# Performance work log

Measured on AMD Instinct MI355X. Metric: run time of the kernel, lower is better.

The kernel has to match this reference:

```python
import jax, jax.numpy as jnp
import numpy as np

N_NODES = 100000
N_EDGES = 3200000
N_GRAPHS = 256
IN_DIM = 128
HID = 64
K = 3


def setup_inputs() -> dict:
    key = jax.random.key(0)
    ks = jax.random.split(key, 10)
    x = jax.random.normal(ks[0], (N_NODES, IN_DIM), dtype=jnp.float32)
    edge_index = jax.random.randint(ks[1], (2, N_EDGES), 0, N_NODES, dtype=jnp.int64)
    batch = jnp.sort(jax.random.randint(ks[2], (N_NODES,), 0, N_GRAPHS, dtype=jnp.int64))
    # ChebConv k-order weights: list of Linear(in, out) -> stacked [K, in, out]
    s1 = 1.0 / np.sqrt(IN_DIM)
    s2 = 1.0 / np.sqrt(HID)
    W1 = jax.random.uniform(ks[3], (K, IN_DIM, HID), jnp.float32, -s1, s1)
    b1 = jax.random.uniform(ks[4], (HID,), jnp.float32, -s1, s1)
    W2 = jax.random.uniform(ks[5], (K, HID, HID), jnp.float32, -s2, s2)
    b2 = jax.random.uniform(ks[6], (HID,), jnp.float32, -s2, s2)
    Wfc = jax.random.uniform(ks[7], (HID, 1), jnp.float32, -s2, s2)
    bfc = jax.random.uniform(ks[8], (1,), jnp.float32, -s2, s2)
    return {"x": x, "edge_index": edge_index, "batch": batch,
            "W1": W1, "b1": b1, "W2": W2, "b2": b2, "Wfc": Wfc, "bfc": bfc}


def _cheb_conv(x, src, dst, edge_w, W, b):
    # PyG ChebConv, sym normalization, lambda_max=2 => L_hat has zero diagonal
    # and off-diagonal -D^{-1/2} A D^{-1/2} (edge_w precomputed, negative).
    n = x.shape[0]
    def lhat(v):  # (L_hat v)_i = sum_{edges j->i} edge_w * v_j
        return jax.ops.segment_sum(edge_w[:, None] * v[src], dst, num_segments=n)
    Tx0 = x
    Tx1 = lhat(Tx0)
    Tx2 = 2.0 * lhat(Tx1) - Tx0
    return Tx0 @ W[0] + Tx1 @ W[1] + Tx2 @ W[2] + b


def reference(x, edge_index, batch, W1, b1, W2, b2, Wfc, bfc):
    src, dst = edge_index[0], edge_index[1]
    n = x.shape[0]
    # degree on row (source), sym normalization
    deg = jax.ops.segment_sum(jnp.ones_like(src, dtype=x.dtype), src, num_segments=n)
    dinv = jnp.where(deg > 0, jax.lax.rsqrt(jnp.maximum(deg, 1.0)), 0.0)
    edge_w = -dinv[src] * dinv[dst]  # scaled Laplacian off-diagonal weights

    h = jax.nn.relu(_cheb_conv(x, src, dst, edge_w, W1, b1))
    h = jax.nn.relu(_cheb_conv(h, src, dst, edge_w, W2, b2))

    # global mean pool over graphs
    sums = jax.ops.segment_sum(h, batch, num_segments=N_GRAPHS)
    counts = jax.ops.segment_sum(jnp.ones((n,), dtype=h.dtype), batch, num_segments=N_GRAPHS)
    pooled = sums / jnp.maximum(counts, 1.0)[:, None]

    return (pooled @ Wfc + bfc).squeeze(-1)  # [N_GRAPHS]
```

## Files before the change

### kernel.cpp

```cpp
#include <hip/hip_runtime.h>
#include <hip/hip_fp16.h>
#include <cstdint>
#include <cstddef>

static constexpr int NN = 100000;
static constexpr int NE = 3200000;
static constexpr int NG = 256;
static constexpr int NBK = (NN + 127) / 128;
static constexpr int EPB = NE / 256;
static constexpr int GB_BATCH = (NN + 255) / 256;
static constexpr int GB_PREPW = (192 * 128 + 192 * 64 + 255) / 256;
static constexpr int GB_HIST = 256;

typedef _Float16 h8 __attribute__((ext_vector_type(8)));
typedef float f4v __attribute__((ext_vector_type(4)));

__device__ __forceinline__ void atomAddF(float* p, float v) {
  unsafeAtomicAdd(p, v);
}
__device__ __forceinline__ float h2f(__half h) { return __half2float(h); }

__global__ void k_detect(const int* __restrict__ ei, int* __restrict__ flag) {
  if (threadIdx.x == 0 && blockIdx.x == 0) {
    int nz = 0;
    for (int i = 0; i < 64; ++i) nz += (ei[2 * i + 1] != 0) ? 1 : 0;
    *flag = (nz == 0) ? 1 : 0;
  }
}

__device__ __forceinline__ int ld_idx(const void* raw, int f, int i) {
  return f ? (int)((const long long*)raw)[i] : ((const int*)raw)[i];
}

__global__ __launch_bounds__(256) void k_front(const void* __restrict__ bat,
                                               const void* __restrict__ ei,
                                               const int* __restrict__ flag,
                                               const float* __restrict__ W1,
                                               const float* __restrict__ W2,
                                               int* __restrict__ b32,
                                               int* __restrict__ gcnt,
                                               __half* __restrict__ BtX,
                                               __half* __restrict__ BtH2,
                                               int* __restrict__ sCnt,
                                               int* __restrict__ dCnt,
                                               int* __restrict__ hsBlk,
                                               int* __restrict__ hdBlk) {
  __shared__ int sh[2 * NBK];
  int b = blockIdx.x;
  int t = threadIdx.x;
  if (b < GB_BATCH) {
    int* cnt = sh;
    cnt[t] = 0;
    int blk0 = b * 256;
    int f = *flag;
    int g0 = ld_idx(bat, f, blk0);
    __syncthreads();
    int i = blk0 + t;
    if (i < NN) {
      int g = ld_idx(bat, f, i);
      b32[i] = g;
      atomicAdd(&cnt[g - g0], 1);
    }
    __syncthreads();
    if (cnt[t] > 0) atomicAdd(&gcnt[g0 + t], cnt[t]);
  } else if (b < GB_BATCH + GB_PREPW) {
    int u = (b - GB_BATCH) * 256 + t;
    if (u < 192 * 128) {
      int n = u >> 7, k = u & 127;
      float v;
      if (n < 64)       v = W1[k * 64 + n] - W1[16384 + k * 64 + n];
      else if (n < 128) v = W1[8192 + k * 64 + (n - 64)];
      else              v = W1[16384 + k * 64 + (n - 128)];
      BtX[n * 128 + k] = __float2half_rn(v);
    } else if (u < 192 * 128 + 192 * 64) {
      int u2 = u - 192 * 128;
      int n = u2 >> 6, k = u2 & 63;
      float v;
      if (n < 64)       v = W2[k * 64 + n] - W2[8192 + k * 64 + n];
      else if (n < 128) v = W2[4096 + k * 64 + (n - 64)];
      else              v = W2[8192 + k * 64 + (n - 128)];
      BtH2[n * 64 + k] = __float2half_rn(v);
    }
  } else {
    int hb = b - GB_BATCH - GB_PREPW;
    int* hs = sh;
    int* hd = sh + NBK;
    for (int i = t; i < NBK; i += 256) { hs[i] = 0; hd[i] = 0; }
    __syncthreads();
    int f = *flag;
    int e0 = hb * EPB;
    for (int e = e0 + t; e < e0 + EPB; e += 256) {
      int s = ld_idx(ei, f, e);
      int d = ld_idx(ei, f, NE + e);
      atomicAdd(&hs[s >> 7], 1);
      atomicAdd(&hd[d >> 7], 1);
    }
    __syncthreads();
    size_t hoff = (size_t)hb * NBK;
    for (int i = t; i < NBK; i += 256) {
      int a = hs[i], c = hd[i];
      hsBlk[hoff + i] = a;
      hdBlk[hoff + i] = c;
      if (a) atomicAdd(&sCnt[i], a);
      if (c) atomicAdd(&dCnt[i], c);
    }
  }
}

__global__ __launch_bounds__(1024) void k_scan(const int* __restrict__ sCnt,
                                               const int* __restrict__ dCnt,
                                               int* __restrict__ sBase,
                                               int* __restrict__ dBase,
                                               int* __restrict__ sCur,
                                               int* __restrict__ dCur) {
  __shared__ int sh1[1024], sh2[1024];
  int t = threadIdx.x;
  int v1 = (t < NBK) ? sCnt[t] : 0;
  int v2 = (t < NBK) ? dCnt[t] : 0;
  sh1[t] = v1; sh2[t] = v2;
  __syncthreads();
  for (int off = 1; off < 1024; off <<= 1) {
    int a1 = (t >= off) ? sh1[t - off] : 0;
    int a2 = (t >= off) ? sh2[t - off] : 0;
    __syncthreads();
    sh1[t] += a1; sh2[t] += a2;
    __syncthreads();
  }
  if (t <= NBK) {
    int b1 = sh1[t] - v1, b2 = sh2[t] - v2;
    sBase[t] = b1; dBase[t] = b2;
    if (t < NBK) { sCur[t] = b1; dCur[t] = b2; }
  }
}

__global__ __launch_bounds__(256) void k_scatter(const void* __restrict__ raw,
                                                 const int* __restrict__ flag,
                                                 const int* __restrict__ hsBlk,
                                                 const int* __restrict__ hdBlk,
                                                 int* __restrict__ sCur,
                                                 int* __restrict__ dCur,
                                                 int* __restrict__ srclist,
                                                 unsigned* __restrict__ elist) {
  __shared__ int hs[NBK], hd[NBK], cbS[NBK], cbD[NBK];
  int t = threadIdx.x;
  size_t hb = (size_t)blockIdx.x * NBK;
  for (int i = t; i < NBK; i += 256) {
    int c1 = hsBlk[hb + i];
    cbS[i] = c1 ? atomicAdd(&sCur[i], c1) : 0;
    int c2 = hdBlk[hb + i];
    cbD[i] = c2 ? atomicAdd(&dCur[i], c2) : 0;
    hs[i] = 0; hd[i] = 0;
  }
  __syncthreads();
  int f = *flag;
  int e0 = blockIdx.x * EPB;
  for (int e = e0 + t; e < e0 + EPB; e += 256) {
    int s = ld_idx(raw, f, e);
    int d = ld_idx(raw, f, NE + e);
    int bs = s >> 7, bd = d >> 7;
    int ls = atomicAdd(&hs[bs], 1);
    int ld2 = atomicAdd(&hd[bd], 1);
    srclist[cbS[bs] + ls] = s;
    elist[cbD[bd] + ld2] = (unsigned)s | ((unsigned)(d & 127) << 17);
  }
}

__global__ __launch_bounds__(256) void k_back(const int* __restrict__ sBase,
                                              const int* __restrict__ srclist,
                                              float* __restrict__ dinv,
                                              const int* __restrict__ dBase,
                                              const unsigned* __restrict__ elist,
                                              int* __restrict__ rowptr,
                                              int* __restrict__ adj) {
  __shared__ int cnt[128], sc[128], off[128], fill[128];
  int t = threadIdx.x;
  int bb = blockIdx.x;
  if (bb < NBK) {
    int b = bb;
    if (t < 128) cnt[t] = 0;
    __syncthreads();
    int e0 = sBase[b], e1 = sBase[b + 1];
    for (int i = e0 + t; i < e1; i += 256) atomicAdd(&cnt[srclist[i] & 127], 1);
    __syncthreads();
    if (t < 128) {
      int node = b * 128 + t;
      if (node < NN) {
        int c = cnt[t];
        dinv[node] = (c > 0) ? rsqrtf((float)c) : 0.f;
      }
    }
  } else {
    int b = bb - NBK;
    if (t < 128) { cnt[t] = 0; fill[t] = 0; }
    __syncthreads();
    int e0 = dBase[b], e1 = dBase[b + 1];
    for (int i = e0 + t; i < e1; i += 256) atomicAdd(&cnt[elist[i] >> 17], 1);
    __syncthreads();
    if (t < 128) sc[t] = cnt[t];
    __syncthreads();
    for (int o = 1; o < 128; o <<= 1) {
      int a = (t < 128 && t >= o) ? sc[t - o] : 0;
      __syncthreads();
      if (t < 128) sc[t] += a;
      __syncthreads();
    }
    if (t < 128) {
      off[t] = sc[t] - cnt[t];
      int node = b * 128 + t;
      if (node < NN) rowptr[node] = e0 + off[t];
    }
    if (b == NBK - 1 && t == 0) rowptr[NN] = e1;
    __syncthreads();
    for (int i = e0 + t; i < e1; i += 256) {
      unsigned w2 = elist[i];
      int l = (int)(w2 >> 17);
      int pos = atomicAdd(&fill[l], 1);
      adj[e0 + off[l] + pos] = (int)(w2 & 0x1FFFFu);
    }
  }
}

static constexpr int AW = 136;
__global__ __launch_bounds__(256) void k_gemm_x(const float* __restrict__ x,
                                                const __half* __restrict__ BtX,
                                                const float* __restrict__ dinv,
                                                __half* __restrict__ gV0,
                                                __half* __restrict__ gA1,
                                                __half* __restrict__ gU2s) {
  __shared__ __align__(16) _Float16 As[128 * AW];
  const int t = threadIdx.x;
  const int n0 = blockIdx.x * 128;
  {
    int i = t >> 1, q = t & 1;
    int row = n0 + i;
    _Float16* dst = As + i * AW + q * 64;
    if (row < NN) {
      const float* src = x + (size_t)row * 128 + q * 64;
#pragma unroll
      for (int c = 0; c < 64; c += 4) {
        float4 v = *reinterpret_cast<const float4*>(src + c);
        ushort4 u;
        u.x = __half_as_ushort(__float2half_rn(v.x));
        u.y = __half_as_ushort(__float2half_rn(v.y));
        u.z = __half_as_ushort(__float2half_rn(v.z));
        u.w = __half_as_ushort(__float2half_rn(v.w));
        *reinterpret_cast<ushort4*>(dst + c) = u;
      }
    } else {
#pragma unroll
      for (int c = 0; c < 64; c += 4)
        *reinterpret_cast<ushort4*>(dst + c) = make_ushort4(0, 0, 0, 0);
    }
  }
  __syncthreads();
  const int w = t >> 6, lane = t & 63;
  const int quad = lane >> 4, l = lane & 15;
  f4v acc[2][12];
#pragma unroll
  for (int mt = 0; mt < 2; ++mt)
#pragma unroll
    for (int nt = 0; nt < 12; ++nt) acc[mt][nt] = (f4v){0.f, 0.f, 0.f, 0.f};

#pragma unroll
  for (int ks = 0; ks < 4; ++ks) {
    int k0 = ks * 32 + quad * 8;
    h8 a0 = *reinterpret_cast<const h8*>(As + (w * 32 + l) * AW + k0);
    h8 a1 = *reinterpret_cast<const h8*>(As + (w * 32 + 16 + l) * AW + k0);
#pragma unroll
    for (int nt = 0; nt < 12; ++nt) {
      h8 b = *reinterpret_cast<const h8*>(BtX + (size_t)(nt * 16 + l) * 128 + k0);
      acc[0][nt] = __builtin_amdgcn_mfma_f32_16x16x32_f16(a0, b, acc[0][nt], 0, 0, 0);
      acc[1][nt] = __builtin_amdgcn_mfma_f32_16x16x32_f16(a1, b, acc[1][nt], 0, 0, 0);
    }
  }
#pragma unroll
  for (int mt = 0; mt < 2; ++mt) {
#pragma unroll
    for (int r = 0; r < 4; ++r) {
      int row = n0 + w * 32 + mt * 16 + quad * 4 + r;
      if (row < NN) {
        float dv = dinv[row];
#pragma unroll
        for (int nt2 = 0; nt2 < 4; ++nt2) {
          int col = nt2 * 16 + l;
          gV0[(size_t)row * 64 + col] = __float2half_rn(acc[mt][nt2][r]);
          gA1[(size_t)row * 64 + col] = __float2half_rn(acc[mt][4 + nt2][r]);
          gU2s[(size_t)row * 64 + col] = __float2half_rn(dv * acc[mt][8 + nt2][r]);
        }
      }
    }
  }
}

static constexpr int HW2 = 72;
__global__ __launch_bounds__(256) void k_gemm_h(const __half* __restrict__ gH1,
                                                const __half* __restrict__ BtH2,
                                                const float* __restrict__ dinv,
                                                __half* __restrict__ gV02,
                                                __half* __restrict__ gA2,
                                                __half* __restrict__ gB2s) {
  __shared__ __align__(16) _Float16 As[128 * HW2];
  const int t = threadIdx.x;
  const int n0 = blockIdx.x * 128;
  for (int c = t; c < 128 * 8; c += 256) {
    int row = c >> 3, seg = c & 7;
    int rowg = n0 + row;
    h8 v = (h8){0, 0, 0, 0, 0, 0, 0, 0};
    if (rowg < NN) v = *reinterpret_cast<const h8*>(gH1 + (size_t)rowg * 64 + seg * 8);
    *reinterpret_cast<h8*>(As + row * HW2 + seg * 8) = v;
  }
  __syncthreads();
  const int w = t >> 6, lane = t & 63;
  const int quad = lane >> 4, l = lane & 15;
  f4v acc[2][12];
#pragma unroll
  for (int mt = 0; mt < 2; ++mt)
#pragma unroll
    for (int nt = 0; nt < 12; ++nt) acc[mt][nt] = (f4v){0.f, 0.f, 0.f, 0.f};
#pragma unroll
  for (int ks = 0; ks < 2; ++ks) {
    int k0 = ks * 32 + quad * 8;
    h8 a0 = *reinterpret_cast<const h8*>(As + (w * 32 + l) * HW2 + k0);
    h8 a1 = *reinterpret_cast<const h8*>(As + (w * 32 + 16 + l) * HW2 + k0);
#pragma unroll
    for (int nt = 0; nt < 12; ++nt) {
      h8 b = *reinterpret_cast<const h8*>(BtH2 + (size_t)(nt * 16 + l) * 64 + k0);
      acc[0][nt] = __builtin_amdgcn_mfma_f32_16x16x32_f16(a0, b, acc[0][nt], 0, 0, 0);
      acc[1][nt] = __builtin_amdgcn_mfma_f32_16x16x32_f16(a1, b, acc[1][nt], 0, 0, 0);
    }
  }
#pragma unroll
  for (int mt = 0; mt < 2; ++mt) {
#pragma unroll
    for (int r = 0; r < 4; ++r) {
      int row = n0 + w * 32 + mt * 16 + quad * 4 + r;
      if (row < NN) {
        float dv = dinv[row];
#pragma unroll
        for (int nt2 = 0; nt2 < 4; ++nt2) {
          int col = nt2 * 16 + l;
          gV02[(size_t)row * 64 + col] = __float2half_rn(acc[mt][nt2][r]);
          gA2[(size_t)row * 64 + col] = __float2half_rn(acc[mt][4 + nt2][r]);
          gB2s[(size_t)row * 64 + col] = __float2half_rn(dv * acc[mt][8 + nt2][r]);
        }
      }
    }
  }
}

#define GATHER_SUM(tbl)                                                    \
  int p0 = rp[node], p1 = rp[node + 1];                                    \
  float a0 = 0.f, a1 = 0.f, a2 = 0.f, a3 = 0.f;                            \
  float a4 = 0.f, a5 = 0.f, a6 = 0.f, a7 = 0.f;                            \
  int p = p0;                                                              \
  int pA = (p0 + 3) & ~3;                                                  \
  if (pA > p1) pA = p1;                                                    \
  for (; p < pA; ++p) a0 += h2f(tbl[(size_t)adj[p] * 64 + d]);             \
  for (; p + 16 <= p1; p += 16) {                                          \
    int4 e0 = *reinterpret_cast<const int4*>(adj + p);                     \
    int4 e1 = *reinterpret_cast<const int4*>(adj + p + 4);                 \
    int4 e2 = *reinterpret_cast<const int4*>(adj + p + 8);                 \
    int4 e3 = *reinterpret_cast<const int4*>(adj + p + 12);                \
    __half v0 = tbl[(size_t)e0.x * 64 + d];                                \
    __half v1 = tbl[(size_t)e0.y * 64 + d];                                \
    __half v2 = tbl[(size_t)e0.z * 64 + d];                                \
    __half v3 = tbl[(size_t)e0.w * 64 + d];                                \
    __half v4 = tbl[(size_t)e1.x * 64 + d];                                \
    __half v5 = tbl[(size_t)e1.y * 64 + d];                                \
    __half v6 = tbl[(size_t)e1.z * 64 + d];                                \
    __half v7 = tbl[(size_t)e1.w * 64 + d];                                \
    __half v8 = tbl[(size_t)e2.x * 64 + d];                                \
    __half v9 = tbl[(size_t)e2.y * 64 + d];                                \
    __half va = tbl[(size_t)e2.z * 64 + d];                                \
    __half vb = tbl[(size_t)e2.w * 64 + d];                                \
    __half vc = tbl[(size_t)e3.x * 64 + d];                                \
    __half vd = tbl[(size_t)e3.y * 64 + d];                                \
    __half ve = tbl[(size_t)e3.z * 64 + d];                                \
    __half vf = tbl[(size_t)e3.w * 64 + d];                                \
    a0 += h2f(v0); a1 += h2f(v1); a2 += h2f(v2); a3 += h2f(v3);            \
    a4 += h2f(v4); a5 += h2f(v5); a6 += h2f(v6); a7 += h2f(v7);            \
    a0 += h2f(v8); a1 += h2f(v9); a2 += h2f(va); a3 += h2f(vb);            \
    a4 += h2f(vc); a5 += h2f(vd); a6 += h2f(ve); a7 += h2f(vf);            \
  }                                                                        \
  if (p + 8 <= p1) {                                                       \
    int4 e0 = *reinterpret_cast<const int4*>(adj + p);                     \
    int4 e1 = *reinterpret_cast<const int4*>(adj + p + 4);                 \
    a0 += h2f(tbl[(size_t)e0.x * 64 + d]);                                 \
    a1 += h2f(tbl[(size_t)e0.y * 64 + d]);                                 \
    a2 += h2f(tbl[(size_t)e0.z * 64 + d]);                                 \
    a3 += h2f(tbl[(size_t)e0.w * 64 + d]);                                 \
    a4 += h2f(tbl[(size_t)e1.x * 64 + d]);                                 \
    a5 += h2f(tbl[(size_t)e1.y * 64 + d]);                                 \
    a6 += h2f(tbl[(size_t)e1.z * 64 + d]);                                 \
    a7 += h2f(tbl[(size_t)e1.w * 64 + d]);                                 \
    p += 8;                                                                \
  }                                                                        \
  if (p + 4 <= p1) {                                                       \
    int4 e = *reinterpret_cast<const int4*>(adj + p);                      \
    a0 += h2f(tbl[(size_t)e.x * 64 + d]);                                  \
    a1 += h2f(tbl[(size_t)e.y * 64 + d]);                                  \
    a2 += h2f(tbl[(size_t)e.z * 64 + d]);                                  \
    a3 += h2f(tbl[(size_t)e.w * 64 + d]);                                  \
    p += 4;                                                                \
  }                                                                        \
  for (; p < p1; ++p) a1 += h2f(tbl[(size_t)adj[p] * 64 + d]);             \
  float s = ((a0 + a1) + (a2 + a3)) + ((a4 + a5) + (a6 + a7));

__global__ __launch_bounds__(256, 8) void k_propA(const int* __restrict__ rp,
                                                  const int* __restrict__ adj,
                                                  const __half* __restrict__ tbl,
                                                  const __half* __restrict__ aux,
                                                  const float* __restrict__ dinv,
                                                  __half* __restrict__ outT) {
  int node = blockIdx.x * 4 + (threadIdx.x >> 6);
  int d = threadIdx.x & 63;
  if (node >= NN) return;
  GATHER_SUM(tbl)
  float dv = dinv[node];
  float tt = -dv * s;
  size_t idx = (size_t)node * 64 + d;
  outT[idx] = __float2half_rn(dv * (h2f(aux[idx]) + 2.f * tt));
}

__global__ __launch_bounds__(256, 8) void k_propB(const int* __restrict__ rp,
                                                  const int* __restrict__ adj,
                                                  const __half* __restrict__ tbl,
                                                  const __half* __restrict__ gV0,
                                                  const float* __restrict__ b1v,
                                                  const float* __restrict__ dinv,
                                                  __half* __restrict__ gH1) {
  int node = blockIdx.x * 4 + (threadIdx.x >> 6);
  int d = threadIdx.x & 63;
  if (node >= NN) return;
  GATHER_SUM(tbl)
  float dv = dinv[node];
  float r = -dv * s;
  size_t idx = (size_t)node * 64 + d;
  float h = fmaxf(h2f(gV0[idx]) + r + b1v[d], 0.f);
  gH1[idx] = __float2half_rn(h);
}

__global__ __launch_bounds__(256, 8) void k_propD(const int* __restrict__ rp,
                                                  const int* __restrict__ adj,
                                                  const __half* __restrict__ tbl,
                                                  const __half* __restrict__ gV02,
                                                  const float* __restrict__ b2v,
                                                  const float* __restrict__ dinv,
                                                  __half* __restrict__ gH2) {
  int node = blockIdx.x * 4 + (threadIdx.x >> 6);
  int d = threadIdx.x & 63;
  if (node >= NN) return;
  GATHER_SUM(tbl)
  float dv = dinv[node];
  float r = -dv * s;
  size_t idx = (size_t)node * 64 + d;
  float h = fmaxf(h2f(gV02[idx]) + r + b2v[d], 0.f);
  gH2[idx] = __float2half_rn(h);
}

__global__ __launch_bounds__(256) void k_pool(const __half* __restrict__ gH2,
                                              const int* __restrict__ b32,
                                              float* __restrict__ pooled) {
  __shared__ int gb[128];
  int t = threadIdx.x;
  int n0 = blockIdx.x * 128;
  if (t < 128) gb[t] = (n0 + t < NN) ? b32[n0 + t] : -1;
  __syncthreads();
  int rg = t >> 6, d = t & 63;
  int base = rg * 32;
  int cur = -2;
  float s = 0.f;
  for (int i = 0; i < 32; ++i) {
    int g = gb[base + i];
    float v = (g >= 0) ? h2f(gH2[(size_t)(n0 + base + i) * 64 + d]) : 0.f;
    if (g != cur) {
      if (cur >= 0) atomAddF(&pooled[cur * 64 + d], s);
      s = 0.f;
      cur = g;
    }
    s += v;
  }
  if (cur >= 0) atomAddF(&pooled[cur * 64 + d], s);
}

__global__ void k_out(const float* __restrict__ pooled, const int* __restrict__ gcnt,
                      const float* __restrict__ Wfc, const float* __restrict__ bfc,
                      float* __restrict__ out) {
  int g = blockIdx.x, t = threadIdx.x;
  float v = pooled[g * 64 + t] * Wfc[t];
  int c = gcnt[g];
  v /= (float)(c > 0 ? c : 1);
  for (int off = 32; off > 0; off >>= 1) v += __shfl_down(v, off, 64);
  if (t == 0) out[g] = v + bfc[0];
}

extern "C" void kernel_launch(void* const* d_in, const int* in_sizes, int n_in,
                              void* d_out, int out_size, void* d_ws, size_t ws_size,
                              hipStream_t stream) {
  const float* x   = (const float*)d_in[0];
  const void*  ei  = d_in[1];
  const void*  bat = d_in[2];
  const float* W1  = (const float*)d_in[3];
  const float* b1v = (const float*)d_in[4];
  const float* W2  = (const float*)d_in[5];
  const float* b2v = (const float*)d_in[6];
  const float* Wfc = (const float*)d_in[7];
  const float* bfc = (const float*)d_in[8];
  float* out = (float*)d_out;

  char* w = (char*)d_ws;
  size_t o = 0;
  auto take = [&](size_t bytes) -> void* {
    void* p = w + o;
    o = (o + bytes + 255) & ~(size_t)255;
    return p;
  };
  int*      flag   = (int*)take(256);
  int*      gcnt   = (int*)take((size_t)NG * 4);
  float*    pooled = (float*)take((size_t)NG * 64 * 4);
  int*      sCnt   = (int*)take((size_t)(NBK + 2) * 4);
  int*      dCnt   = (int*)take((size_t)(NBK + 2) * 4);
  char*     zend   = w + o;
  int*      sBase  = (int*)take((size_t)(NBK + 2) * 4);
  int*      dBase  = (int*)take((size_t)(NBK + 2) * 4);
  int*      sCur   = (int*)take((size_t)(NBK + 2) * 4);
  int*      dCur   = (int*)take((size_t)(NBK + 2) * 4);
  int*      b32    = (int*)take((size_t)NN * 4);
  float*    dinv   = (float*)take((size_t)NN * 4);
  int*      rowptr = (int*)take((size_t)(NN + 2) * 4);
  int*      hsBlk  = (int*)take((size_t)256 * NBK * 4);
  int*      hdBlk  = (int*)take((size_t)256 * NBK * 4);
  int*      srclist= (int*)take((size_t)NE * 4);
  unsigned* elist  = (unsigned*)take((size_t)NE * 4);
  int*      adj    = (int*)take((size_t)NE * 4);
  __half*   BtX    = (__half*)take((size_t)192 * 128 * 2);
  __half*   BtH2   = (__half*)take((size_t)192 * 64 * 2);
  __half*   gV0    = (__half*)take((size_t)NN * 64 * 2);
  __half*   gA1    = (__half*)take((size_t)NN * 64 * 2);
  __half*   gU2s   = (__half*)take((size_t)NN * 64 * 2);
  __half*   gM1    = (__half*)take((size_t)NN * 64 * 2);
  __half*   gH1    = (__half*)take((size_t)NN * 64 * 2);
  __half*   gV02   = gU2s;
  __half*   gA2    = gA1;
  __half*   gB2s   = gV0;
  __half*   gM2    = gM1;
  __half*   gH2    = gH1;
  (void)in_sizes; (void)n_in; (void)out_size; (void)ws_size;

  hipMemsetAsync(gcnt, 0, (size_t)(zend - (char*)gcnt), stream);

  k_detect<<<1, 64, 0, stream>>>((const int*)ei, flag);
  k_front<<<GB_BATCH + GB_PREPW + GB_HIST, 256, 0, stream>>>(
      bat, ei, flag, W1, W2, b32, gcnt, BtX, BtH2, sCnt, dCnt, hsBlk, hdBlk);
  k_scan<<<1, 1024, 0, stream>>>(sCnt, dCnt, sBase, dBase, sCur, dCur);
  k_scatter<<<256, 256, 0, stream>>>(ei, flag, hsBlk, hdBlk, sCur, dCur, srclist, elist);
  k_back<<<2 * NBK, 256, 0, stream>>>(sBase, srclist, dinv, dBase, elist, rowptr, adj);

  const int gemm_grid = (NN + 127) / 128;
  const int prop_grid = (NN + 3) / 4;

  k_gemm_x<<<gemm_grid, 256, 0, stream>>>(x, BtX, dinv, gV0, gA1, gU2s);
  k_propA<<<prop_grid, 256, 0, stream>>>(rowptr, adj, gU2s, gA1, dinv, gM1);
  k_propB<<<prop_grid, 256, 0, stream>>>(rowptr, adj, gM1, gV0, b1v, dinv, gH1);
  k_gemm_h<<<gemm_grid, 256, 0, stream>>>(gH1, BtH2, dinv, gV02, gA2, gB2s);
  k_propA<<<prop_grid, 256, 0, stream>>>(rowptr, adj, gB2s, gA2, dinv, gM2);
  k_propD<<<prop_grid, 256, 0, stream>>>(rowptr, adj, gM2, gV02, b2v, dinv, gH2);
  k_pool<<<NBK, 256, 0, stream>>>(gH2, b32, pooled);
  k_out<<<NG, 64, 0, stream>>>(pooled, gcnt, Wfc, bfc, out);
}
```

Measured before the change: 626.3 us.

## Gather half2 pairs per lane and split neighbor lists across half-wavefronts

Each wavefront still handles one node, but each lane now loads a __half2, covering two feature columns, instead of a single half. The two 32-lane halves take disjoint halves of the neighbor list and combine their sums with a cross-lane shuffle. The adjacency list now stores byte offsets (index<<7) so the gather computes addresses with 32-bit adds and no multiply. This aims to raise bytes per load instruction and cut address math, at the cost of more registers (occupancy hint lowered from 8 to 6) and half the lanes sitting idle in the epilogue.

```diff
diff --git a/kernel.cpp b/kernel.cpp
--- a/kernel.cpp
+++ b/kernel.cpp
@@ -215,7 +215,7 @@
       unsigned w2 = elist[i];
       int l = (int)(w2 >> 17);
       int pos = atomicAdd(&fill[l], 1);
-      adj[e0 + off[l] + pos] = (int)(w2 & 0x1FFFFu);
+      adj[e0 + off[l] + pos] = (int)((w2 & 0x1FFFFu) << 7);
     }
   }
 }
@@ -348,114 +348,159 @@
   }
 }
 
-#define GATHER_SUM(tbl)                                                    \
-  int p0 = rp[node], p1 = rp[node + 1];                                    \
-  float a0 = 0.f, a1 = 0.f, a2 = 0.f, a3 = 0.f;                            \
-  float a4 = 0.f, a5 = 0.f, a6 = 0.f, a7 = 0.f;                            \
-  int p = p0;                                                              \
-  int pA = (p0 + 3) & ~3;                                                  \
-  if (pA > p1) pA = p1;                                                    \
-  for (; p < pA; ++p) a0 += h2f(tbl[(size_t)adj[p] * 64 + d]);             \
-  for (; p + 16 <= p1; p += 16) {                                          \
-    int4 e0 = *reinterpret_cast<const int4*>(adj + p);                     \
-    int4 e1 = *reinterpret_cast<const int4*>(adj + p + 4);                 \
-    int4 e2 = *reinterpret_cast<const int4*>(adj + p + 8);                 \
-    int4 e3 = *reinterpret_cast<const int4*>(adj + p + 12);                \
-    __half v0 = tbl[(size_t)e0.x * 64 + d];                                \
-    __half v1 = tbl[(size_t)e0.y * 64 + d];                                \
-    __half v2 = tbl[(size_t)e0.z * 64 + d];                                \
-    __half v3 = tbl[(size_t)e0.w * 64 + d];                                \
-    __half v4 = tbl[(size_t)e1.x * 64 + d];                                \
-    __half v5 = tbl[(size_t)e1.y * 64 + d];                                \
-    __half v6 = tbl[(size_t)e1.z * 64 + d];                                \
-    __half v7 = tbl[(size_t)e1.w * 64 + d];                                \
-    __half v8 = tbl[(size_t)e2.x * 64 + d];                                \
-    __half v9 = tbl[(size_t)e2.y * 64 + d];                                \
-    __half va = tbl[(size_t)e2.z * 64 + d];                                \
-    __half vb = tbl[(size_t)e2.w * 64 + d];                                \
-    __half vc = tbl[(size_t)e3.x * 64 + d];                                \
-    __half vd = tbl[(size_t)e3.y * 64 + d];                                \
-    __half ve = tbl[(size_t)e3.z * 64 + d];                                \
-    __half vf = tbl[(size_t)e3.w * 64 + d];                                \
-    a0 += h2f(v0); a1 += h2f(v1); a2 += h2f(v2); a3 += h2f(v3);            \
-    a4 += h2f(v4); a5 += h2f(v5); a6 += h2f(v6); a7 += h2f(v7);            \
-    a0 += h2f(v8); a1 += h2f(v9); a2 += h2f(va); a3 += h2f(vb);            \
-    a4 += h2f(vc); a5 += h2f(vd); a6 += h2f(ve); a7 += h2f(vf);            \
-  }                                                                        \
-  if (p + 8 <= p1) {                                                       \
-    int4 e0 = *reinterpret_cast<const int4*>(adj + p);                     \
-    int4 e1 = *reinterpret_cast<const int4*>(adj + p + 4);                 \
-    a0 += h2f(tbl[(size_t)e0.x * 64 + d]);                                 \
-    a1 += h2f(tbl[(size_t)e0.y * 64 + d]);                                 \
-    a2 += h2f(tbl[(size_t)e0.z * 64 + d]);                                 \
-    a3 += h2f(tbl[(size_t)e0.w * 64 + d]);                                 \
-    a4 += h2f(tbl[(size_t)e1.x * 64 + d]);                                 \
-    a5 += h2f(tbl[(size_t)e1.y * 64 + d]);                                 \
-    a6 += h2f(tbl[(size_t)e1.z * 64 + d]);                                 \
-    a7 += h2f(tbl[(size_t)e1.w * 64 + d]);                                 \
-    p += 8;                                                                \
-  }                                                                        \
-  if (p + 4 <= p1) {                                                       \
-    int4 e = *reinterpret_cast<const int4*>(adj + p);                      \
-    a0 += h2f(tbl[(size_t)e.x * 64 + d]);                                  \
-    a1 += h2f(tbl[(size_t)e.y * 64 + d]);                                  \
-    a2 += h2f(tbl[(size_t)e.z * 64 + d]);                                  \
-    a3 += h2f(tbl[(size_t)e.w * 64 + d]);                                  \
-    p += 4;                                                                \
-  }                                                                        \
-  for (; p < p1; ++p) a1 += h2f(tbl[(size_t)adj[p] * 64 + d]);             \
-  float s = ((a0 + a1) + (a2 + a3)) + ((a4 + a5) + (a6 + a7));
-
-__global__ __launch_bounds__(256, 8) void k_propA(const int* __restrict__ rp,
+__device__ __forceinline__ __half2 ld2(const char* tb, unsigned off) {
+  return *reinterpret_cast<const __half2*>(tb + off);
+}
+__device__ __forceinline__ void acc2(float2& a, __half2 v) {
+  float2 f = __half22float2(v);
+  a.x += f.x;
+  a.y += f.y;
+}
+
+#define GATHER_SUM2(TBL)                                                      \
+  const char* tb = reinterpret_cast<const char*>(TBL);                        \
+  int q0 = rp[node], q1 = rp[node + 1];                                       \
+  int pm = q0 + ((q1 - q0 + 1) >> 1);                                         \
+  int p = half ? pm : q0;                                                     \
+  int p1 = half ? q1 : pm;                                                    \
+  float2 A0 = make_float2(0.f, 0.f), A1 = A0, A2 = A0, A3 = A0;               \
+  float2 A4 = A0, A5 = A0, A6 = A0, A7 = A0;                                  \
+  int pA = (p + 3) & ~3;                                                      \
+  if (pA > p1) pA = p1;                                                       \
+  for (; p < pA; ++p) acc2(A0, ld2(tb, (unsigned)adj[p] + d4));               \
+  for (; p + 16 <= p1; p += 16) {                                             \
+    int4 e0 = *reinterpret_cast<const int4*>(adj + p);                        \
+    int4 e1 = *reinterpret_cast<const int4*>(adj + p + 4);                    \
+    int4 e2 = *reinterpret_cast<const int4*>(adj + p + 8);                    \
+    int4 e3 = *reinterpret_cast<const int4*>(adj + p + 12);                   \
+    __half2 v0 = ld2(tb, (unsigned)e0.x + d4);                                \
+    __half2 v1 = ld2(tb, (unsigned)e0.y + d4);                                \
+    __half2 v2 = ld2(tb, (unsigned)e0.z + d4);                                \
+    __half2 v3 = ld2(tb, (unsigned)e0.w + d4);                                \
+    __half2 v4 = ld2(tb, (unsigned)e1.x + d4);                                \
+    __half2 v5 = ld2(tb, (unsigned)e1.y + d4);                                \
+    __half2 v6 = ld2(tb, (unsigned)e1.z + d4);                                \
+    __half2 v7 = ld2(tb, (unsigned)e1.w + d4);                                \
+    __half2 v8 = ld2(tb, (unsigned)e2.x + d4);                                \
+    __half2 v9 = ld2(tb, (unsigned)e2.y + d4);                                \
+    __half2 va = ld2(tb, (unsigned)e2.z + d4);                                \
+    __half2 vb = ld2(tb, (unsigned)e2.w + d4);                                \
+    __half2 vc = ld2(tb, (unsigned)e3.x + d4);                                \
+    __half2 vd = ld2(tb, (unsigned)e3.y + d4);                                \
+    __half2 ve = ld2(tb, (unsigned)e3.z + d4);                                \
+    __half2 vf = ld2(tb, (unsigned)e3.w + d4);                                \
+    acc2(A0, v0); acc2(A1, v1); acc2(A2, v2); acc2(A3, v3);                   \
+    acc2(A4, v4); acc2(A5, v5); acc2(A6, v6); acc2(A7, v7);                   \
+    acc2(A0, v8); acc2(A1, v9); acc2(A2, va); acc2(A3, vb);                   \
+    acc2(A4, vc); acc2(A5, vd); acc2(A6, ve); acc2(A7, vf);                   \
+  }                                                                           \
+  if (p + 8 <= p1) {                                                          \
+    int4 e0 = *reinterpret_cast<const int4*>(adj + p);                        \
+    int4 e1 = *reinterpret_cast<const int4*>(adj + p + 4);                    \
+    __half2 v0 = ld2(tb, (unsigned)e0.x + d4);                                \
+    __half2 v1 = ld2(tb, (unsigned)e0.y + d4);                                \
+    __half2 v2 = ld2(tb, (unsigned)e0.z + d4);                                \
+    __half2 v3 = ld2(tb, (unsigned)e0.w + d4);                                \
+    __half2 v4 = ld2(tb, (unsigned)e1.x + d4);                                \
+    __half2 v5 = ld2(tb, (unsigned)e1.y + d4);                                \
+    __half2 v6 = ld2(tb, (unsigned)e1.z + d4);                                \
+    __half2 v7 = ld2(tb, (unsigned)e1.w + d4);                                \
+    acc2(A0, v0); acc2(A1, v1); acc2(A2, v2); acc2(A3, v3);                   \
+    acc2(A4, v4); acc2(A5, v5); acc2(A6, v6); acc2(A7, v7);                   \
+    p += 8;                                                                   \
+  }                                                                           \
+  if (p + 4 <= p1) {                                                          \
+    int4 e = *reinterpret_cast<const int4*>(adj + p);                         \
+    __half2 v0 = ld2(tb, (unsigned)e.x + d4);                                 \
+    __half2 v1 = ld2(tb, (unsigned)e.y + d4);                                 \
+    __half2 v2 = ld2(tb, (unsigned)e.z + d4);                                 \
+    __half2 v3 = ld2(tb, (unsigned)e.w + d4);                                 \
+    acc2(A0, v0); acc2(A1, v1); acc2(A2, v2); acc2(A3, v3);                   \
+    p += 4;                                                                   \
+  }                                                                           \
+  for (; p < p1; ++p) acc2(A1, ld2(tb, (unsigned)adj[p] + d4));               \
+  float2 S;                                                                   \
+  S.x = ((A0.x + A1.x) + (A2.x + A3.x)) + ((A4.x + A5.x) + (A6.x + A7.x));    \
+  S.y = ((A0.y + A1.y) + (A2.y + A3.y)) + ((A4.y + A5.y) + (A6.y + A7.y));    \
+  S.x += __shfl_xor(S.x, 32);                                                 \
+  S.y += __shfl_xor(S.y, 32);
+
+__global__ __launch_bounds__(256, 6) void k_propA(const int* __restrict__ rp,
                                                   const int* __restrict__ adj,
                                                   const __half* __restrict__ tbl,
                                                   const __half* __restrict__ aux,
                                                   const float* __restrict__ dinv,
                                                   __half* __restrict__ outT) {
-  int node = blockIdx.x * 4 + (threadIdx.x >> 6);
-  int d = threadIdx.x & 63;
+  int t = threadIdx.x;
+  int node = blockIdx.x * 4 + (t >> 6);
+  int half = (t >> 5) & 1;
+  int l = t & 31;
+  unsigned d4 = (unsigned)l * 4;
+  int d2 = l * 2;
   if (node >= NN) return;
-  GATHER_SUM(tbl)
-  float dv = dinv[node];
-  float tt = -dv * s;
-  size_t idx = (size_t)node * 64 + d;
-  outT[idx] = __float2half_rn(dv * (h2f(aux[idx]) + 2.f * tt));
-}
-
-__global__ __launch_bounds__(256, 8) void k_propB(const int* __restrict__ rp,
+  GATHER_SUM2(tbl)
+  if (half == 0) {
+    float dv = dinv[node];
+    float tx = -dv * S.x, ty = -dv * S.y;
+    size_t idx = (size_t)node * 64 + d2;
+    float2 af = __half22float2(*reinterpret_cast<const __half2*>(aux + idx));
+    *reinterpret_cast<__half2*>(outT + idx) =
+        __floats2half2_rn(dv * (af.x + 2.f * tx), dv * (af.y + 2.f * ty));
+  }
+}
+
+__global__ __launch_bounds__(256, 6) void k_propB(const int* __restrict__ rp,
                                                   const int* __restrict__ adj,
                                                   const __half* __restrict__ tbl,
                                                   const __half* __restrict__ gV0,
                                                   const float* __restrict__ b1v,
                                                   const float* __restrict__ dinv,
                                                   __half* __restrict__ gH1) {
-  int node = blockIdx.x * 4 + (threadIdx.x >> 6);
-  int d = threadIdx.x & 63;
+  int t = threadIdx.x;
+  int node = blockIdx.x * 4 + (t >> 6);
+  int half = (t >> 5) & 1;
+  int l = t & 31;
+  unsigned d4 = (unsigned)l * 4;
+  int d2 = l * 2;
   if (node >= NN) return;
-  GATHER_SUM(tbl)
-  float dv = dinv[node];
-  float r = -dv * s;
-  size_t idx = (size_t)node * 64 + d;
-  float h = fmaxf(h2f(gV0[idx]) + r + b1v[d], 0.f);
-  gH1[idx] = __float2half_rn(h);
-}
-
-__global__ __launch_bounds__(256, 8) void k_propD(const int* __restrict__ rp,
+  GATHER_SUM2(tbl)
+  if (half == 0) {
+    float dv = dinv[node];
+    float rx = -dv * S.x, ry = -dv * S.y;
+    size_t idx = (size_t)node * 64 + d2;
+    float2 vf0 = __half22float2(*reinterpret_cast<const __half2*>(gV0 + idx));
+    float2 bb = *reinterpret_cast<const float2*>(b1v + d2);
+    *reinterpret_cast<__half2*>(gH1 + idx) =
+        __floats2half2_rn(fmaxf(vf0.x + rx + bb.x, 0.f),
+                          fmaxf(vf0.y + ry + bb.y, 0.f));
+  }
+}
+
+__global__ __launch_bounds__(256, 6) void k_propD(const int* __restrict__ rp,
                                                   const int* __restrict__ adj,
                                                   const __half* __restrict__ tbl,
                                                   const __half* __restrict__ gV02,
                                                   const float* __restrict__ b2v,
                                                   const float* __restrict__ dinv,
                                                   __half* __restrict__ gH2) {
-  int node = blockIdx.x * 4 + (threadIdx.x >> 6);
-  int d = threadIdx.x & 63;
+  int t = threadIdx.x;
+  int node = blockIdx.x * 4 + (t >> 6);
+  int half = (t >> 5) & 1;
+  int l = t & 31;
+  unsigned d4 = (unsigned)l * 4;
+  int d2 = l * 2;
   if (node >= NN) return;
-  GATHER_SUM(tbl)
-  float dv = dinv[node];
-  float r = -dv * s;
-  size_t idx = (size_t)node * 64 + d;
-  float h = fmaxf(h2f(gV02[idx]) + r + b2v[d], 0.f);
-  gH2[idx] = __float2half_rn(h);
+  GATHER_SUM2(tbl)
+  if (half == 0) {
+    float dv = dinv[node];
+    float rx = -dv * S.x, ry = -dv * S.y;
+    size_t idx = (size_t)node * 64 + d2;
+    float2 vf0 = __half22float2(*reinterpret_cast<const __half2*>(gV02 + idx));
+    float2 bb = *reinterpret_cast<const float2*>(b2v + d2);
+    *reinterpret_cast<__half2*>(gH2 + idx) =
+        __floats2half2_rn(fmaxf(vf0.x + rx + bb.x, 0.f),
+                          fmaxf(vf0.y + ry + bb.y, 0.f));
+  }
 }
 
 __global__ __launch_bounds__(256) void k_pool(const __half* __restrict__ gH2,
```

Result: no change. 626.0 us (-0.0%).
